# Optimization experiments

Measured on AMD Instinct MI355X. Metric: run time of the kernel, lower is better.

The kernel has to match this reference:

```python
import jax, jax.numpy as jnp
import numpy as np

N = 50000      # nodes
E = 800000     # edges
F_IN = 64      # num_node_features
H = 128        # hidden_channels
C = 2          # num_classes
G = 16         # graphs in batch


def setup_inputs() -> dict:
    key = jax.random.key(0)
    ks = jax.random.split(key, 16)
    def lin(k, fan_in, shape):
        return jax.random.normal(k, shape, jnp.float32) / np.sqrt(fan_in)
    return {
        "x": jax.random.normal(ks[0], (N, F_IN), jnp.float32),
        "edge_index": jax.random.randint(ks[1], (2, E), 0, N, dtype=jnp.int32),
        "batch": jnp.sort(jax.random.randint(ks[2], (N,), 0, G, dtype=jnp.int32)),
        "W1": lin(ks[3], F_IN, (F_IN, H)), "b1": jnp.zeros((H,), jnp.float32),
        "W2": lin(ks[4], H, (H, H)),       "b2": jnp.zeros((H,), jnp.float32),
        "W3": lin(ks[5], H, (H, H)),       "b3": jnp.zeros((H,), jnp.float32),
        "W4": lin(ks[6], H, (H, H)),       "b4": jnp.zeros((H,), jnp.float32),
        "lw1": lin(ks[7], H, (H, H // 2)), "lb1": jnp.zeros((H // 2,), jnp.float32),
        "lw2": lin(ks[8], H // 2, (H // 2, C)), "lb2": jnp.zeros((C,), jnp.float32),
    }


def _graph_norm(edge_index):
    # PyG GCNConv default: add self-loops, symmetric normalization.
    loop = jnp.arange(N, dtype=edge_index.dtype)
    src = jnp.concatenate([edge_index[0], loop])  # message source
    dst = jnp.concatenate([edge_index[1], loop])  # aggregation target
    deg = jax.ops.segment_sum(jnp.ones_like(dst, jnp.float32), dst, num_segments=N)
    dinv = jnp.where(deg > 0, jax.lax.rsqrt(deg), 0.0)
    norm = dinv[src] * dinv[dst]                  # [E+N]
    return src, dst, norm


def _gcn_conv(h, W, b, src, dst, norm):
    hw = h @ W                                    # [N, out]
    msg = hw[src] * norm[:, None]                 # gather + normalize  [E+N, out]
    agg = jax.ops.segment_sum(msg, dst, num_segments=N)  # scatter-add
    return agg + b


def reference(x, edge_index, batch, W1, b1, W2, b2, W3, b3, W4, b4, lw1, lb1, lw2, lb2):
    src, dst, norm = _graph_norm(edge_index)
    h = jax.nn.relu(_gcn_conv(x, W1, b1, src, dst, norm))   # dropout inactive (eval)
    h = jax.nn.relu(_gcn_conv(h, W2, b2, src, dst, norm))
    h = jax.nn.relu(_gcn_conv(h, W3, b3, src, dst, norm))
    h = _gcn_conv(h, W4, b4, src, dst, norm)
    # global_mean_pool over graph ids
    cnt = jax.ops.segment_sum(jnp.ones((N,), jnp.float32), batch, num_segments=G)
    pooled = jax.ops.segment_sum(h, batch, num_segments=G) / jnp.maximum(cnt, 1.0)[:, None]
    out = jax.nn.relu(pooled @ lw1 + lb1)
    return out @ lw2 + lb2
```

## Files before the change

### kernel.cpp

```cpp
#include <hip/hip_runtime.h>

#define NN 50000
#define NPAD 50048
#define NE 800000
#define FIN 64
#define H 128
#define NG 16
#define POOL_BLOCKS 1000
#define POOL_NODES 50
#define NPART 64
#define NBUCK 196
#define BUCK_CAP 4800
#define FILLA_BLOCKS 512
#define FILLA_CHUNK 1563
#define CHUNK_U 16
#define DUMMY NN
#define AGG_CH (NPAD / 64)
#define ZERO_I4 33024
#define PREP_ITEMS (NPAD * FIN + H * FIN + 3 * H * H + ZERO_I4)
#define PREP_BLOCKS ((PREP_ITEMS + 255) / 256)

typedef __bf16 bf16x8 __attribute__((ext_vector_type(8)));
typedef float f32x4 __attribute__((ext_vector_type(4)));
typedef float f32x2 __attribute__((ext_vector_type(2)));

__device__ inline unsigned short bf16r(float x) {
    unsigned int u = __float_as_uint(x);
    return (unsigned short)((u + 0x7fffu + ((u >> 16) & 1u)) >> 16);
}
__device__ inline unsigned int pack_bf16x2(float a, float b) {
    return (unsigned int)bf16r(a) | ((unsigned int)bf16r(b) << 16);
}
__device__ inline float bf_lo(unsigned int u) { return __uint_as_float(u << 16); }
__device__ inline float bf_hi(unsigned int u) { return __uint_as_float(u & 0xffff0000u); }

__device__ inline void pkadd(f32x2& a, unsigned int u) {
    f32x2 p;
    p.x = bf_lo(u);
    p.y = bf_hi(u);
    asm("v_pk_add_f32 %0, %1, %0" : "+v"(a) : "v"(p));
}

__global__ __launch_bounds__(256) void fillA_prep_kernel(const int* __restrict__ ei,
                                                         int* __restrict__ gcount,
                                                         unsigned int* __restrict__ ebuf,
                                                         const float* __restrict__ x,
                                                         const float* __restrict__ W1,
                                                         const float* __restrict__ W2,
                                                         const float* __restrict__ W3,
                                                         const float* __restrict__ W4,
                                                         unsigned short* __restrict__ xb,
                                                         unsigned short* __restrict__ Wt1,
                                                         unsigned short* __restrict__ Wt2,
                                                         unsigned short* __restrict__ Wt3,
                                                         unsigned short* __restrict__ Wt4,
                                                         int4* __restrict__ zbuf) {
    const int t = threadIdx.x;
    if (blockIdx.x >= FILLA_BLOCKS) {
        int e = (blockIdx.x - FILLA_BLOCKS) * 256 + t;
        if (e < NPAD * FIN) {
            int n = e >> 6, k = e & 63;
            unsigned short v = (n < NN) ? bf16r(x[n * FIN + k]) : (unsigned short)0;
            xb[(size_t)(k >> 5) * (NPAD * 32) + n * 32 + (k & 31)] = v;
            return;
        }
        int tt = e - NPAD * FIN;
        if (tt < H * FIN) {
            int n = tt / FIN, k = tt % FIN;
            Wt1[tt] = bf16r(W1[k * H + n]);
            return;
        }
        int u = tt - H * FIN;
        if (u < 3 * H * H) {
            const float* W = W2;
            unsigned short* Wt = Wt2;
            if (u >= 2 * H * H) { W = W4; Wt = Wt4; u -= 2 * H * H; }
            else if (u >= H * H) { W = W3; Wt = Wt3; u -= H * H; }
            int n = u / H, k = u % H;
            Wt[u] = bf16r(W[k * H + n]);
            return;
        }
        int z = u - 3 * H * H;
        if (z < ZERO_I4) zbuf[z] = make_int4(0, 0, 0, 0);
        return;
    }
    __shared__ int hist[256];
    __shared__ int base[256];
    hist[t] = 0;
    __syncthreads();
    const int e0 = blockIdx.x * FILLA_CHUNK;
    const int e1 = min(e0 + FILLA_CHUNK, NE);
    for (int e = e0 + t; e < e1; e += 256)
        atomicAdd(&hist[ei[NE + e] >> 8], 1);
    __syncthreads();
    {
        int h = hist[t];
        base[t] = h ? atomicAdd(&gcount[t], h) : 0;
    }
    __syncthreads();
    for (int e = e0 + t; e < e1; e += 256) {
        int d = ei[NE + e];
        int s = ei[e];
        int b = d >> 8;
        int pos = atomicAdd(&base[b], 1);
        ebuf[b * BUCK_CAP + pos] = (unsigned int)s | ((unsigned int)d << 16);
    }
}

__global__ __launch_bounds__(256) void fillB_kernel(const unsigned int* __restrict__ ebuf,
                                                    const int* __restrict__ gcount,
                                                    int* __restrict__ galloc,
                                                    int2* __restrict__ rowse,
                                                    float* __restrict__ dinv,
                                                    unsigned short* __restrict__ csr) {
    __shared__ int lh[256];
    __shared__ int lsum[256];
    __shared__ int lcur[256];
    __shared__ int base_s;
    const int b = blockIdx.x, t = threadIdx.x;
    const int n0 = b * 256;
    lh[t] = 0;
    __syncthreads();
    const int ne = gcount[b];
    const unsigned int* __restrict__ eb = ebuf + b * BUCK_CAP;
    for (int i = t; i < ne; i += 256)
        atomicAdd(&lh[(int)(eb[i] >> 16) - n0], 1);
    __syncthreads();
    const int c = lh[t];
    const int p = (c + 7) & ~7;
    lsum[t] = p;
    __syncthreads();
    for (int off = 1; off < 256; off <<= 1) {
        int u = (t >= off) ? lsum[t - off] : 0;
        __syncthreads();
        lsum[t] += u;
        __syncthreads();
    }
    if (t == 255) base_s = atomicAdd(galloc, lsum[255]);
    const int excl = t ? lsum[t - 1] : 0;
    __syncthreads();
    const int st = base_s + excl;
    const int n = n0 + t;
    if (n < NN) {
        rowse[n] = make_int2(st, st + p);
        dinv[n] = rsqrtf((float)c + 1.0f);
    } else if (n < NPAD) {
        rowse[n] = make_int2(0, 0);
        dinv[n] = 0.0f;
    }
    lcur[t] = st;
    __syncthreads();
    for (int i = t; i < ne; i += 256) {
        unsigned int u = eb[i];
        int pos = atomicAdd(&lcur[(int)(u >> 16) - n0], 1);
        csr[pos] = (unsigned short)(u & 0xFFFFu);
    }
    __syncthreads();
    for (int k = st + c; k < st + p; k++) csr[k] = (unsigned short)DUMMY;
}

#define LSTRIDE 130
template <int K>
__global__ __launch_bounds__(256) void gemm_mfma_kernel(const unsigned short* __restrict__ hb,
                                                        const unsigned short* __restrict__ Wt,
                                                        const float* __restrict__ dinv,
                                                        unsigned int* __restrict__ outu) {
    __shared__ float ls[64 * LSTRIDE];
    const int wave = threadIdx.x >> 6, lane = threadIdx.x & 63;
    const int m15 = lane & 15, quad = lane >> 4;
    const int row0 = blockIdx.x * 64;
    const int arow = row0 + wave * 16 + m15;

    bf16x8 a[K / 32];
#pragma unroll
    for (int ks = 0; ks < K / 32; ks++)
        a[ks] = *(const bf16x8*)&hb[(size_t)ks * (NPAD * 32) + arow * 32 + quad * 8];

    const int lrow = wave * 16 + quad * 4;
    float dv[4];
#pragma unroll
    for (int r = 0; r < 4; r++) dv[r] = dinv[row0 + lrow + r];

#pragma unroll
    for (int ct = 0; ct < 8; ct++) {
        f32x4 acc = {0.f, 0.f, 0.f, 0.f};
#pragma unroll
        for (int ks = 0; ks < K / 32; ks++) {
            bf16x8 b = *(const bf16x8*)&Wt[(ct * 16 + m15) * K + ks * 32 + quad * 8];
            acc = __builtin_amdgcn_mfma_f32_16x16x32_bf16(a[ks], b, acc, 0, 0, 0);
        }
#pragma unroll
        for (int r = 0; r < 4; r++)
            ls[(lrow + r) * LSTRIDE + ct * 16 + m15] = acc[r] * dv[r];
    }
    __syncthreads();

#pragma unroll
    for (int k = 0; k < 4; k++) {
        int idx = threadIdx.x + 256 * k;
        int c = idx >> 8, row = (idx >> 2) & 63, q = idx & 3;
        const float* p = &ls[row * LSTRIDE + c * 32 + q * 8];
        uint4 o;
        o.x = pack_bf16x2(p[0], p[1]);
        o.y = pack_bf16x2(p[2], p[3]);
        o.z = pack_bf16x2(p[4], p[5]);
        o.w = pack_bf16x2(p[6], p[7]);
        *(uint4*)&outu[(size_t)c * (NPAD * CHUNK_U) + (size_t)(row0 + row) * CHUNK_U + q * 4] = o;
    }
}

template <bool RELU_BIAS>
__global__ __launch_bounds__(256) void agg_kernel(const unsigned int* __restrict__ hwc,
                                                  const int2* __restrict__ rowse,
                                                  const unsigned short* __restrict__ csr,
                                                  const float* __restrict__ dinv,
                                                  const float* __restrict__ bias,
                                                  unsigned int* __restrict__ outc) {
    const int chunk = blockIdx.x / AGG_CH;
    const int nb = blockIdx.x % AGG_CH;
    const int g = threadIdx.x & 3;
    const int n = nb * 64 + (threadIdx.x >> 2);
    const int u0 = g * 4;
    const unsigned int* __restrict__ slice = hwc + (size_t)chunk * (NPAD * CHUNK_U);

    uint4 sv = *(const uint4*)&slice[n * CHUNK_U + u0];
    f32x2 a0 = {bf_lo(sv.x), bf_hi(sv.x)};
    f32x2 a1 = {bf_lo(sv.y), bf_hi(sv.y)};
    f32x2 a2 = {bf_lo(sv.z), bf_hi(sv.z)};
    f32x2 a3 = {bf_lo(sv.w), bf_hi(sv.w)};

    const int2 se = rowse[n];
    for (int i = se.x; i < se.y; i += 8) {
        uint4 c = *(const uint4*)&csr[i];
        int s0 = c.x & 0xFFFF, s1 = c.x >> 16;
        int s2 = c.y & 0xFFFF, s3 = c.y >> 16;
        int s4 = c.z & 0xFFFF, s5 = c.z >> 16;
        int s6 = c.w & 0xFFFF, s7 = c.w >> 16;
        uint4 v0 = *(const uint4*)&slice[s0 * CHUNK_U + u0];
        uint4 v1 = *(const uint4*)&slice[s1 * CHUNK_U + u0];
        uint4 v2 = *(const uint4*)&slice[s2 * CHUNK_U + u0];
        uint4 v3 = *(const uint4*)&slice[s3 * CHUNK_U + u0];
        uint4 v4 = *(const uint4*)&slice[s4 * CHUNK_U + u0];
        uint4 v5 = *(const uint4*)&slice[s5 * CHUNK_U + u0];
        uint4 v6 = *(const uint4*)&slice[s6 * CHUNK_U + u0];
        uint4 v7 = *(const uint4*)&slice[s7 * CHUNK_U + u0];
        pkadd(a0, v0.x); pkadd(a1, v0.y); pkadd(a2, v0.z); pkadd(a3, v0.w);
        pkadd(a0, v1.x); pkadd(a1, v1.y); pkadd(a2, v1.z); pkadd(a3, v1.w);
        pkadd(a0, v2.x); pkadd(a1, v2.y); pkadd(a2, v2.z); pkadd(a3, v2.w);
        pkadd(a0, v3.x); pkadd(a1, v3.y); pkadd(a2, v3.z); pkadd(a3, v3.w);
        pkadd(a0, v4.x); pkadd(a1, v4.y); pkadd(a2, v4.z); pkadd(a3, v4.w);
        pkadd(a0, v5.x); pkadd(a1, v5.y); pkadd(a2, v5.z); pkadd(a3, v5.w);
        pkadd(a0, v6.x); pkadd(a1, v6.y); pkadd(a2, v6.z); pkadd(a3, v6.w);
        pkadd(a0, v7.x); pkadd(a1, v7.y); pkadd(a2, v7.z); pkadd(a3, v7.w);
    }

    const float d = dinv[n];
    uint4 o;
    if (RELU_BIAS) {
        const float2* bp = (const float2*)bias + chunk * CHUNK_U + u0;
        float2 q0 = bp[0], q1 = bp[1], q2 = bp[2], q3 = bp[3];
        o.x = pack_bf16x2(fmaxf(a0.x * d + q0.x, 0.f), fmaxf(a0.y * d + q0.y, 0.f));
        o.y = pack_bf16x2(fmaxf(a1.x * d + q1.x, 0.f), fmaxf(a1.y * d + q1.y, 0.f));
        o.z = pack_bf16x2(fmaxf(a2.x * d + q2.x, 0.f), fmaxf(a2.y * d + q2.y, 0.f));
        o.w = pack_bf16x2(fmaxf(a3.x * d + q3.x, 0.f), fmaxf(a3.y * d + q3.y, 0.f));
    } else {
        o.x = pack_bf16x2(a0.x * d, a0.y * d);
        o.y = pack_bf16x2(a1.x * d, a1.y * d);
        o.z = pack_bf16x2(a2.x * d, a2.y * d);
        o.w = pack_bf16x2(a3.x * d, a3.y * d);
    }
    *(uint4*)&outc[(size_t)chunk * (NPAD * CHUNK_U) + (size_t)n * CHUNK_U + u0] = o;
}

__global__ __launch_bounds__(256) void pool_kernel(const unsigned int* __restrict__ hbu,
                                                   const float* __restrict__ b4,
                                                   const int* __restrict__ batch,
                                                   float* __restrict__ poolpart,
                                                   float* __restrict__ pcntpart) {
    __shared__ int bs[POOL_NODES];
    const int tid = threadIdx.x;
    const int n0 = blockIdx.x * POOL_NODES;
    if (tid < POOL_NODES) bs[tid] = batch[n0 + tid];
    __syncthreads();
    float* __restrict__ pooled = poolpart + (blockIdx.x & (NPART - 1)) * (NG * H);
    float* __restrict__ cnt = pcntpart + (blockIdx.x & (NPART - 1)) * NG;
    const int c2 = tid & 63;
    const int chunk = c2 >> 4, u = c2 & 15;
    const int rsub = tid >> 6;
    float2 bb = ((const float2*)b4)[c2];
    float2 acc = {0.f, 0.f};
    float cacc = 0.f;
    int curg = bs[rsub];
    const size_t coff = (size_t)chunk * (NPAD * CHUNK_U) + u;
    for (int r = rsub; r < POOL_NODES; r += 4) {
        int g = bs[r];
        if (g != curg) {
            atomicAdd(&pooled[curg * H + c2 * 2], acc.x);
            atomicAdd(&pooled[curg * H + c2 * 2 + 1], acc.y);
            if (c2 == 0) atomicAdd(&cnt[curg], cacc);
            acc.x = acc.y = 0.f;
            cacc = 0.f;
            curg = g;
        }
        unsigned int v = hbu[coff + (size_t)(n0 + r) * CHUNK_U];
        acc.x += bf_lo(v) + bb.x;
        acc.y += bf_hi(v) + bb.y;
        cacc += 1.f;
    }
    atomicAdd(&pooled[curg * H + c2 * 2], acc.x);
    atomicAdd(&pooled[curg * H + c2 * 2 + 1], acc.y);
    if (c2 == 0) atomicAdd(&cnt[curg], cacc);
}

__global__ __launch_bounds__(1024) void mlp_kernel(const float* __restrict__ poolpart,
                                                   const float* __restrict__ pcntpart,
                                                   const float* __restrict__ lw1,
                                                   const float* __restrict__ lb1,
                                                   const float* __restrict__ lw2,
                                                   const float* __restrict__ lb2,
                                                   float* __restrict__ out) {
    __shared__ float mean_s[NG * H];
    __shared__ float cnt_s[NG];
    __shared__ float hid_s[NG * 64];
    int tid = threadIdx.x;
    if (tid < NG) {
        float c = 0.f;
        for (int p = 0; p < NPART; p++) c += pcntpart[p * NG + tid];
        cnt_s[tid] = fmaxf(c, 1.0f);
    }
    __syncthreads();
    for (int i = tid; i < NG * H; i += 1024) {
        float s = 0.f;
        for (int p = 0; p < NPART; p++) s += poolpart[p * (NG * H) + i];
        mean_s[i] = s / cnt_s[i >> 7];
    }
    __syncthreads();
    {
        int g = tid >> 6, j = tid & 63;
        float acc = lb1[j];
        for (int f = 0; f < H; f++) acc += mean_s[g * H + f] * lw1[f * 64 + j];
        hid_s[g * 64 + j] = fmaxf(acc, 0.f);
    }
    __syncthreads();
    if (tid < 32) {
        int g = tid >> 1, c = tid & 1;
        float acc = lb2[c];
        for (int j = 0; j < 64; j++) acc += hid_s[g * 64 + j] * lw2[j * 2 + c];
        out[g * 2 + c] = acc;
    }
}

extern "C" void kernel_launch(void* const* d_in, const int* in_sizes, int n_in,
                              void* d_out, int out_size, void* d_ws, size_t ws_size,
                              hipStream_t stream) {
    const float* x = (const float*)d_in[0];
    const int* ei = (const int*)d_in[1];
    const int* batch = (const int*)d_in[2];
    const float* W1 = (const float*)d_in[3];
    const float* b1 = (const float*)d_in[4];
    const float* W2 = (const float*)d_in[5];
    const float* b2 = (const float*)d_in[6];
    const float* W3 = (const float*)d_in[7];
    const float* b3 = (const float*)d_in[8];
    const float* W4 = (const float*)d_in[9];
    const float* b4 = (const float*)d_in[10];
    const float* lw1 = (const float*)d_in[11];
    const float* lb1 = (const float*)d_in[12];
    const float* lw2 = (const float*)d_in[13];
    const float* lb2 = (const float*)d_in[14];
    float* out = (float*)d_out;

    int* wsi = (int*)d_ws;
    int* gcount = wsi;
    int* galloc = wsi + 256;
    float* poolpart = (float*)(wsi + 512);
    float* pcntpart = (float*)(wsi + 131584);
    int2* rowse = (int2*)(wsi + 132608);
    unsigned short* csr = (unsigned short*)(wsi + 232704);
    float* dinv = (float*)(wsi + 832704);
    unsigned short* Wt1 = (unsigned short*)(wsi + 882752);
    unsigned short* Wt2 = (unsigned short*)(wsi + 886848);
    unsigned short* Wt3 = (unsigned short*)(wsi + 895040);
    unsigned short* Wt4 = (unsigned short*)(wsi + 903232);
    unsigned short* xb = (unsigned short*)(wsi + 911424);
    unsigned int* hb = (unsigned int*)(wsi + 2512960);
    unsigned int* hwb = (unsigned int*)(wsi + 5716032);
    unsigned int* ebuf = (unsigned int*)(wsi + 8919104);

    const int gemmBlocks = NPAD / 64;
    const int aggBlocks = 4 * AGG_CH;

    hipMemsetAsync(wsi, 0, 512 * sizeof(int), stream);
    fillA_prep_kernel<<<FILLA_BLOCKS + PREP_BLOCKS, 256, 0, stream>>>(
        ei, gcount, ebuf, x, W1, W2, W3, W4, xb, Wt1, Wt2, Wt3, Wt4, (int4*)poolpart);
    fillB_kernel<<<NBUCK, 256, 0, stream>>>(ebuf, gcount, galloc, rowse, dinv, csr);

    gemm_mfma_kernel<FIN><<<gemmBlocks, 256, 0, stream>>>(xb, Wt1, dinv, hwb);
    agg_kernel<true><<<aggBlocks, 256, 0, stream>>>(hwb, rowse, csr, dinv, b1, hb);
    gemm_mfma_kernel<H><<<gemmBlocks, 256, 0, stream>>>((unsigned short*)hb, Wt2, dinv, hwb);
    agg_kernel<true><<<aggBlocks, 256, 0, stream>>>(hwb, rowse, csr, dinv, b2, hb);
    gemm_mfma_kernel<H><<<gemmBlocks, 256, 0, stream>>>((unsigned short*)hb, Wt3, dinv, hwb);
    agg_kernel<true><<<aggBlocks, 256, 0, stream>>>(hwb, rowse, csr, dinv, b3, hb);
    gemm_mfma_kernel<H><<<gemmBlocks, 256, 0, stream>>>((unsigned short*)hb, Wt4, dinv, hwb);
    agg_kernel<false><<<aggBlocks, 256, 0, stream>>>(hwb, rowse, csr, dinv, nullptr, hb);

    pool_kernel<<<POOL_BLOCKS, 256, 0, stream>>>(hb, b4, batch, poolpart, pcntpart);
    mlp_kernel<<<1, 1024, 0, stream>>>(poolpart, pcntpart, lw1, lb1, lw2, lb2, out);
}
```

Measured before the change: 334.2 us.

## Sort nodes by degree class for aggregation and fuse mean-pool into final aggregation

Nodes are bucketed by padded degree class during CSR build, and a permutation is written in the first GEMM so that aggregation threads in a wave process nodes of similar degree, which reduces divergence from uneven row lengths. The last aggregation pass now atomically accumulates its per-node results directly into pooled partial sums, which removes the separate pool kernel and the write/read of the final hidden layer. Graph counts are computed once in fillB, and the b4 bias is added after the mean. The cost is scattered per-node output stores in the earlier aggregation layers and many float atomics in the last one.

Result: slower. 634.4 us (+89.8%).

```diff
diff --git a/kernel.cpp b/kernel.cpp
--- a/kernel.cpp
+++ b/kernel.cpp
@@ -6,8 +6,6 @@
 #define FIN 64
 #define H 128
 #define NG 16
-#define POOL_BLOCKS 1000
-#define POOL_NODES 50
 #define NPART 64
 #define NBUCK 196
 #define BUCK_CAP 4800
@@ -16,7 +14,7 @@
 #define CHUNK_U 16
 #define DUMMY NN
 #define AGG_CH (NPAD / 64)
-#define ZERO_I4 33024
+#define ZERO_I4 32768
 #define PREP_ITEMS (NPAD * FIN + H * FIN + 3 * H * H + ZERO_I4)
 #define PREP_BLOCKS ((PREP_ITEMS + 255) / 256)
 
@@ -110,16 +108,24 @@
 __global__ __launch_bounds__(256) void fillB_kernel(const unsigned int* __restrict__ ebuf,
                                                     const int* __restrict__ gcount,
                                                     int* __restrict__ galloc,
+                                                    int* __restrict__ classCnt,
+                                                    int* __restrict__ pcnt,
+                                                    const int* __restrict__ batch,
                                                     int2* __restrict__ rowse,
                                                     float* __restrict__ dinv,
+                                                    int* __restrict__ nclass,
                                                     unsigned short* __restrict__ csr) {
     __shared__ int lh[256];
     __shared__ int lsum[256];
     __shared__ int lcur[256];
+    __shared__ int lcls[16];
+    __shared__ int lclsbase[16];
+    __shared__ int lgc[16];
     __shared__ int base_s;
     const int b = blockIdx.x, t = threadIdx.x;
     const int n0 = b * 256;
     lh[t] = 0;
+    if (t < 16) { lcls[t] = 0; lgc[t] = 0; }
     __syncthreads();
     const int ne = gcount[b];
     const unsigned int* __restrict__ eb = ebuf + b * BUCK_CAP;
@@ -128,8 +134,19 @@
     __syncthreads();
     const int c = lh[t];
     const int p = (c + 7) & ~7;
+    const int n = n0 + t;
+    int cls = 0, lrank = 0;
+    if (n < NN) {
+        cls = min(p >> 3, 15);
+        lrank = atomicAdd(&lcls[cls], 1);
+        atomicAdd(&lgc[batch[n]], 1);
+    }
     lsum[t] = p;
     __syncthreads();
+    if (t < 16) {
+        lclsbase[t] = lcls[t] ? atomicAdd(&classCnt[t], lcls[t]) : 0;
+        if (lgc[t]) atomicAdd(&pcnt[t], lgc[t]);
+    }
     for (int off = 1; off < 256; off <<= 1) {
         int u = (t >= off) ? lsum[t - off] : 0;
         __syncthreads();
@@ -140,10 +157,10 @@
     const int excl = t ? lsum[t - 1] : 0;
     __syncthreads();
     const int st = base_s + excl;
-    const int n = n0 + t;
     if (n < NN) {
         rowse[n] = make_int2(st, st + p);
         dinv[n] = rsqrtf((float)c + 1.0f);
+        nclass[n] = (lclsbase[cls] + lrank) | (cls << 24);
     } else if (n < NPAD) {
         rowse[n] = make_int2(0, 0);
         dinv[n] = 0.0f;
@@ -160,16 +177,33 @@
 }
 
 #define LSTRIDE 130
-template <int K>
+template <int K, bool PERM>
 __global__ __launch_bounds__(256) void gemm_mfma_kernel(const unsigned short* __restrict__ hb,
                                                         const unsigned short* __restrict__ Wt,
                                                         const float* __restrict__ dinv,
+                                                        const int* __restrict__ nclass,
+                                                        const int* __restrict__ classCnt,
+                                                        int* __restrict__ perm,
                                                         unsigned int* __restrict__ outu) {
     __shared__ float ls[64 * LSTRIDE];
     const int wave = threadIdx.x >> 6, lane = threadIdx.x & 63;
     const int m15 = lane & 15, quad = lane >> 4;
     const int row0 = blockIdx.x * 64;
     const int arow = row0 + wave * 16 + m15;
+
+    if (PERM && threadIdx.x < 64) {
+        int n = row0 + threadIdx.x;
+        if (n < NN) {
+            int pk = nclass[n];
+            int cls = pk >> 24, rk = pk & 0xFFFFFF;
+            int base = 0;
+#pragma unroll
+            for (int j = 0; j < 16; j++) base += (j < cls) ? classCnt[j] : 0;
+            perm[base + rk] = n;
+        } else {
+            perm[n] = n;
+        }
+    }
 
     bf16x8 a[K / 32];
 #pragma unroll
@@ -209,17 +243,22 @@
     }
 }
 
-template <bool RELU_BIAS>
+template <int MODE>
 __global__ __launch_bounds__(256) void agg_kernel(const unsigned int* __restrict__ hwc,
                                                   const int2* __restrict__ rowse,
                                                   const unsigned short* __restrict__ csr,
                                                   const float* __restrict__ dinv,
                                                   const float* __restrict__ bias,
+                                                  const int* __restrict__ perm,
+                                                  const int* __restrict__ batch,
+                                                  float* __restrict__ poolpart,
                                                   unsigned int* __restrict__ outc) {
     const int chunk = blockIdx.x / AGG_CH;
     const int nb = blockIdx.x % AGG_CH;
     const int g = threadIdx.x & 3;
-    const int n = nb * 64 + (threadIdx.x >> 2);
+    const int slot = nb * 64 + (threadIdx.x >> 2);
+    const int n = perm[slot];
+    if (MODE == 1 && n >= NN) return;
     const int u0 = g * 4;
     const unsigned int* __restrict__ slice = hwc + (size_t)chunk * (NPAD * CHUNK_U);
 
@@ -255,65 +294,33 @@
     }
 
     const float d = dinv[n];
+    if (MODE == 1) {
+        const int gr = batch[n];
+        float* __restrict__ pp =
+            poolpart + (nb & (NPART - 1)) * (NG * H) + gr * H + chunk * 32 + u0 * 2;
+        atomicAdd(&pp[0], a0.x * d);
+        atomicAdd(&pp[1], a0.y * d);
+        atomicAdd(&pp[2], a1.x * d);
+        atomicAdd(&pp[3], a1.y * d);
+        atomicAdd(&pp[4], a2.x * d);
+        atomicAdd(&pp[5], a2.y * d);
+        atomicAdd(&pp[6], a3.x * d);
+        atomicAdd(&pp[7], a3.y * d);
+        return;
+    }
+    const float2* bp = (const float2*)bias + chunk * CHUNK_U + u0;
+    float2 q0 = bp[0], q1 = bp[1], q2 = bp[2], q3 = bp[3];
     uint4 o;
-    if (RELU_BIAS) {
-        const float2* bp = (const float2*)bias + chunk * CHUNK_U + u0;
-        float2 q0 = bp[0], q1 = bp[1], q2 = bp[2], q3 = bp[3];
-        o.x = pack_bf16x2(fmaxf(a0.x * d + q0.x, 0.f), fmaxf(a0.y * d + q0.y, 0.f));
-        o.y = pack_bf16x2(fmaxf(a1.x * d + q1.x, 0.f), fmaxf(a1.y * d + q1.y, 0.f));
-        o.z = pack_bf16x2(fmaxf(a2.x * d + q2.x, 0.f), fmaxf(a2.y * d + q2.y, 0.f));
-        o.w = pack_bf16x2(fmaxf(a3.x * d + q3.x, 0.f), fmaxf(a3.y * d + q3.y, 0.f));
-    } else {
-        o.x = pack_bf16x2(a0.x * d, a0.y * d);
-        o.y = pack_bf16x2(a1.x * d, a1.y * d);
-        o.z = pack_bf16x2(a2.x * d, a2.y * d);
-        o.w = pack_bf16x2(a3.x * d, a3.y * d);
-    }
+    o.x = pack_bf16x2(fmaxf(a0.x * d + q0.x, 0.f), fmaxf(a0.y * d + q0.y, 0.f));
+    o.y = pack_bf16x2(fmaxf(a1.x * d + q1.x, 0.f), fmaxf(a1.y * d + q1.y, 0.f));
+    o.z = pack_bf16x2(fmaxf(a2.x * d + q2.x, 0.f), fmaxf(a2.y * d + q2.y, 0.f));
+    o.w = pack_bf16x2(fmaxf(a3.x * d + q3.x, 0.f), fmaxf(a3.y * d + q3.y, 0.f));
     *(uint4*)&outc[(size_t)chunk * (NPAD * CHUNK_U) + (size_t)n * CHUNK_U + u0] = o;
 }
 
-__global__ __launch_bounds__(256) void pool_kernel(const unsigned int* __restrict__ hbu,
+__global__ __launch_bounds__(1024) void mlp_kernel(const float* __restrict__ poolpart,
+                                                   const int* __restrict__ pcnt,
                                                    const float* __restrict__ b4,
-                                                   const int* __restrict__ batch,
-                                                   float* __restrict__ poolpart,
-                                                   float* __restrict__ pcntpart) {
-    __shared__ int bs[POOL_NODES];
-    const int tid = threadIdx.x;
-    const int n0 = blockIdx.x * POOL_NODES;
-    if (tid < POOL_NODES) bs[tid] = batch[n0 + tid];
-    __syncthreads();
-    float* __restrict__ pooled = poolpart + (blockIdx.x & (NPART - 1)) * (NG * H);
-    float* __restrict__ cnt = pcntpart + (blockIdx.x & (NPART - 1)) * NG;
-    const int c2 = tid & 63;
-    const int chunk = c2 >> 4, u = c2 & 15;
-    const int rsub = tid >> 6;
-    float2 bb = ((const float2*)b4)[c2];
-    float2 acc = {0.f, 0.f};
-    float cacc = 0.f;
-    int curg = bs[rsub];
-    const size_t coff = (size_t)chunk * (NPAD * CHUNK_U) + u;
-    for (int r = rsub; r < POOL_NODES; r += 4) {
-        int g = bs[r];
-        if (g != curg) {
-            atomicAdd(&pooled[curg * H + c2 * 2], acc.x);
-            atomicAdd(&pooled[curg * H + c2 * 2 + 1], acc.y);
-            if (c2 == 0) atomicAdd(&cnt[curg], cacc);
-            acc.x = acc.y = 0.f;
-            cacc = 0.f;
-            curg = g;
-        }
-        unsigned int v = hbu[coff + (size_t)(n0 + r) * CHUNK_U];
-        acc.x += bf_lo(v) + bb.x;
-        acc.y += bf_hi(v) + bb.y;
-        cacc += 1.f;
-    }
-    atomicAdd(&pooled[curg * H + c2 * 2], acc.x);
-    atomicAdd(&pooled[curg * H + c2 * 2 + 1], acc.y);
-    if (c2 == 0) atomicAdd(&cnt[curg], cacc);
-}
-
-__global__ __launch_bounds__(1024) void mlp_kernel(const float* __restrict__ poolpart,
-                                                   const float* __restrict__ pcntpart,
                                                    const float* __restrict__ lw1,
                                                    const float* __restrict__ lb1,
                                                    const float* __restrict__ lw2,
@@ -323,16 +330,12 @@
     __shared__ float cnt_s[NG];
     __shared__ float hid_s[NG * 64];
     int tid = threadIdx.x;
-    if (tid < NG) {
-        float c = 0.f;
-        for (int p = 0; p < NPART; p++) c += pcntpart[p * NG + tid];
-        cnt_s[tid] = fmaxf(c, 1.0f);
-    }
+    if (tid < NG) cnt_s[tid] = fmaxf((float)pcnt[tid], 1.0f);
     __syncthreads();
     for (int i = tid; i < NG * H; i += 1024) {
         float s = 0.f;
         for (int p = 0; p < NPART; p++) s += poolpart[p * (NG * H) + i];
-        mean_s[i] = s / cnt_s[i >> 7];
+        mean_s[i] = s / cnt_s[i >> 7] + b4[i & (H - 1)];
     }
     __syncthreads();
     {
@@ -373,19 +376,22 @@
     int* wsi = (int*)d_ws;
     int* gcount = wsi;
     int* galloc = wsi + 256;
+    int* classCnt = wsi + 264;
+    int* pcnt = wsi + 280;
     float* poolpart = (float*)(wsi + 512);
-    float* pcntpart = (float*)(wsi + 131584);
-    int2* rowse = (int2*)(wsi + 132608);
-    unsigned short* csr = (unsigned short*)(wsi + 232704);
-    float* dinv = (float*)(wsi + 832704);
-    unsigned short* Wt1 = (unsigned short*)(wsi + 882752);
-    unsigned short* Wt2 = (unsigned short*)(wsi + 886848);
-    unsigned short* Wt3 = (unsigned short*)(wsi + 895040);
-    unsigned short* Wt4 = (unsigned short*)(wsi + 903232);
-    unsigned short* xb = (unsigned short*)(wsi + 911424);
-    unsigned int* hb = (unsigned int*)(wsi + 2512960);
-    unsigned int* hwb = (unsigned int*)(wsi + 5716032);
-    unsigned int* ebuf = (unsigned int*)(wsi + 8919104);
+    int2* rowse = (int2*)(wsi + 131584);
+    unsigned short* csr = (unsigned short*)(wsi + 231680);
+    float* dinv = (float*)(wsi + 831680);
+    unsigned short* Wt1 = (unsigned short*)(wsi + 881728);
+    unsigned short* Wt2 = (unsigned short*)(wsi + 885824);
+    unsigned short* Wt3 = (unsigned short*)(wsi + 894016);
+    unsigned short* Wt4 = (unsigned short*)(wsi + 902208);
+    unsigned short* xb = (unsigned short*)(wsi + 910400);
+    unsigned int* hb = (unsigned int*)(wsi + 2511936);
+    unsigned int* hwb = (unsigned int*)(wsi + 5715008);
+    unsigned int* ebuf = (unsigned int*)(wsi + 8918080);
+    int* nclass = wsi + 9858880;
+    int* perm = wsi + 9908928;
 
     const int gemmBlocks = NPAD / 64;
     const int aggBlocks = 4 * AGG_CH;
@@ -393,17 +399,25 @@
     hipMemsetAsync(wsi, 0, 512 * sizeof(int), stream);
     fillA_prep_kernel<<<FILLA_BLOCKS + PREP_BLOCKS, 256, 0, stream>>>(
         ei, gcount, ebuf, x, W1, W2, W3, W4, xb, Wt1, Wt2, Wt3, Wt4, (int4*)poolpart);
-    fillB_kernel<<<NBUCK, 256, 0, stream>>>(ebuf, gcount, galloc, rowse, dinv, csr);
-
-    gemm_mfma_kernel<FIN><<<gemmBlocks, 256, 0, stream>>>(xb, Wt1, dinv, hwb);
-    agg_kernel<true><<<aggBlocks, 256, 0, stream>>>(hwb, rowse, csr, dinv, b1, hb);
-    gemm_mfma_kernel<H><<<gemmBlocks, 256, 0, stream>>>((unsigned short*)hb, Wt2, dinv, hwb);
-    agg_kernel<true><<<aggBlocks, 256, 0, stream>>>(hwb, rowse, csr, dinv, b2, hb);
-    gemm_mfma_kernel<H><<<gemmBlocks, 256, 0, stream>>>((unsigned short*)hb, Wt3, dinv, hwb);
-    agg_kernel<true><<<aggBlocks, 256, 0, stream>>>(hwb, rowse, csr, dinv, b3, hb);
-    gemm_mfma_kernel<H><<<gemmBlocks, 256, 0, stream>>>((unsigned short*)hb, Wt4, dinv, hwb);
-    agg_kernel<false><<<aggBlocks, 256, 0, stream>>>(hwb, rowse, csr, dinv, nullptr, hb);
-
-    pool_kernel<<<POOL_BLOCKS, 256, 0, stream>>>(hb, b4, batch, poolpart, pcntpart);
-    mlp_kernel<<<1, 1024, 0, stream>>>(poolpart, pcntpart, lw1, lb1, lw2, lb2, out);
-}
+    fillB_kernel<<<NBUCK, 256, 0, stream>>>(ebuf, gcount, galloc, classCnt, pcnt, batch,
+                                            rowse, dinv, nclass, csr);
+
+    gemm_mfma_kernel<FIN, true><<<gemmBlocks, 256, 0, stream>>>(xb, Wt1, dinv, nclass,
+                                                                classCnt, perm, hwb);
+    agg_kernel<0><<<aggBlocks, 256, 0, stream>>>(hwb, rowse, csr, dinv, b1, perm, batch,
+                                                 nullptr, hb);
+    gemm_mfma_kernel<H, false><<<gemmBlocks, 256, 0, stream>>>((unsigned short*)hb, Wt2, dinv,
+                                                               nullptr, nullptr, nullptr, hwb);
+    agg_kernel<0><<<aggBlocks, 256, 0, stream>>>(hwb, rowse, csr, dinv, b2, perm, batch,
+                                                 nullptr, hb);
+    gemm_mfma_kernel<H, false><<<gemmBlocks, 256, 0, stream>>>((unsigned short*)hb, Wt3, dinv,
+                                                               nullptr, nullptr, nullptr, hwb);
+    agg_kernel<0><<<aggBlocks, 256, 0, stream>>>(hwb, rowse, csr, dinv, b3, perm, batch,
+                                                 nullptr, hb);
+    gemm_mfma_kernel<H, false><<<gemmBlocks, 256, 0, stream>>>((unsigned short*)hb, Wt4, dinv,
+                                                               nullptr, nullptr, nullptr, hwb);
+    agg_kernel<1><<<aggBlocks, 256, 0, stream>>>(hwb, rowse, csr, dinv, nullptr, perm, batch,
+                                                 poolpart, nullptr);
+
+    mlp_kernel<<<1, 1024, 0, stream>>>(poolpart, pcnt, b4, lw1, lb1, lw2, lb2, out);
+}
```
